# Kernel tuning notes

Measured on AMD Instinct MI355X. Metric: run time of the kernel, lower is better.

## Reference

```python
import jax, jax.numpy as jnp
import numpy as np

LAMBDA_INIT = 0.8
EPS = 1e-5


def setup_inputs() -> dict:
    key = jax.random.key(0)
    k1, k2, k3, k4 = jax.random.split(key, 4)
    B, H, S, D = 2, 16, 2048, 64
    return {
        "query": jax.random.normal(k1, (B, H, S, D), dtype=jnp.float32),
        "key": jax.random.normal(k2, (B, H, S, D), dtype=jnp.float32),
        "value": jax.random.normal(k3, (B, H, S, D), dtype=jnp.float32),
        "lambda_params": jax.random.uniform(k4, (H,), dtype=jnp.float32),
    }


def reference(query, key, value, lambda_params):
    # query/key/value: [B, H, S, D]; lambda_params: [H]
    B, H, S, D = query.shape
    d2 = D // 2
    scale = 1.0 / jnp.sqrt(jnp.float32(d2))
    q1, q2 = query[..., :d2], query[..., d2:]
    k1, k2 = key[..., :d2], key[..., d2:]
    # Two softmax attention maps over the split halves: [B, H, Sq, Sk]
    a1 = jax.nn.softmax(jnp.einsum("bhqd,bhkd->bhqk", q1, k1) * scale, axis=-1)
    a2 = jax.nn.softmax(jnp.einsum("bhqd,bhkd->bhqk", q2, k2) * scale, axis=-1)
    lam = lambda_params[None, :, None, None]  # [1, H, 1, 1]
    attn = a1 - lam * a2
    out = jnp.einsum("bhqk,bhkd->bhqd", attn, value)  # [B, H, S, D]
    # Groupnorm-style normalization per (batch, head, position) over head_dim,
    # then rescale by (1 - lambda_init).
    mean = jnp.mean(out, axis=-1, keepdims=True)
    var = jnp.mean(jnp.square(out - mean), axis=-1, keepdims=True)
    out = (out - mean) * jax.lax.rsqrt(var + EPS)
    out = out * (1.0 - LAMBDA_INIT)
    return out
```

## Files before the change

### kernel.cpp

```cpp
#include <hip/hip_runtime.h>

typedef __bf16 bf16x8 __attribute__((ext_vector_type(8)));
typedef float f32x4 __attribute__((ext_vector_type(4)));

static __device__ __forceinline__ f32x4 mfma16(bf16x8 a, bf16x8 b, f32x4 c) {
  return __builtin_amdgcn_mfma_f32_16x16x32_bf16(a, b, c, 0, 0, 0);
}
static __device__ __forceinline__ unsigned cvtpk(float lo, float hi) {
  unsigned r;
  asm("v_cvt_pk_bf16_f32 %0, %1, %2" : "=v"(r) : "v"(lo), "v"(hi));
  return r;
}

__global__ __launch_bounds__(256)
void kpack(const float* __restrict__ K, __bf16* __restrict__ KS) {
  const int bh = blockIdx.x >> 6, ch = blockIdx.x & 63;
  const int t = threadIdx.x;
  const int t2 = t >> 7, br = (t >> 6) & 1, g = (t >> 4) & 3, c = t & 15;
  const float* src = K + ((size_t)bh * 2048 + ch * 32 + t2 * 16 + c) * 64 + br * 32 + g * 8;
  float4 f0 = *(const float4*)src;
  float4 f1 = *(const float4*)(src + 4);
  bf16x8 v;
  v[0] = (__bf16)f0.x; v[1] = (__bf16)f0.y; v[2] = (__bf16)f0.z; v[3] = (__bf16)f0.w;
  v[4] = (__bf16)f1.x; v[5] = (__bf16)f1.y; v[6] = (__bf16)f1.z; v[7] = (__bf16)f1.w;
  *(bf16x8*)(KS + (size_t)bh * 131072 + ch * 2048 + t * 8) = v;
}

__global__ __launch_bounds__(256)
void vpack(const float* __restrict__ V, __bf16* __restrict__ VS) {
  __shared__ float tile[64][65];
  const int bh = blockIdx.x >> 5;
  const int s0 = (blockIdx.x & 31) * 64;
  const int t = threadIdx.x;
  const float* Vb = V + (size_t)bh * 2048 * 64;
#pragma unroll
  for (int i = 0; i < 4; ++i) {
    const int r = i * 16 + (t >> 4);
    const int c4 = (t & 15) * 4;
    float4 v = *(const float4*)(Vb + (s0 + r) * 64 + c4);
    tile[r][c4] = v.x; tile[r][c4 + 1] = v.y;
    tile[r][c4 + 2] = v.z; tile[r][c4 + 3] = v.w;
  }
  __syncthreads();
  const int dt = t >> 6, g = (t >> 4) & 3, c = t & 15;
#pragma unroll
  for (int h = 0; h < 2; ++h) {
    const int ch = (blockIdx.x & 31) * 2 + h;
    bf16x8 v;
#pragma unroll
    for (int j = 0; j < 8; ++j) v[j] = (__bf16)tile[h * 32 + 8 * g + j][16 * dt + c];
    *(bf16x8*)(VS + (size_t)bh * 131072 + ch * 2048 + dt * 512 + g * 128 + c * 8) = v;
  }
}

__global__ __launch_bounds__(256, 2)
void diffattn(const float* __restrict__ Q, const __bf16* __restrict__ KS,
              const __bf16* __restrict__ VS, const float* __restrict__ LP,
              float* __restrict__ OUT) {
  constexpr int S = 2048, D = 64;
  constexpr float QSCALE = 0.17677669529663687f * 1.4426950408889634f;

  __shared__ __align__(16) unsigned short Pl[4][2][16][40];

  const int raw = blockIdx.x;
  const int wg  = (raw & 7) * 64 + (raw >> 3);
  const int bh  = wg >> 4;
  const int qb  = wg & 15;
  const float lam = LP[bh & 15];

  const int tid  = threadIdx.x;
  const int w    = tid >> 6;
  const int lane = tid & 63;
  const int c    = lane & 15;
  const int g    = lane >> 4;
  const int q0   = qb * 128 + w * 32;

  const float*  Qb    = Q  + (size_t)bh * S * D;
  const __bf16* Kbase = KS + (size_t)bh * 131072 + g * 128 + c * 8;
  const __bf16* Vbase = VS + (size_t)bh * 131072 + g * 128 + c * 8;

  bf16x8 bq[2][2];
#pragma unroll
  for (int qt = 0; qt < 2; ++qt)
#pragma unroll
    for (int br = 0; br < 2; ++br) {
      const float* p = Qb + (q0 + qt * 16 + c) * D + br * 32 + 8 * g;
      float4 f0 = *(const float4*)p;
      float4 f1 = *(const float4*)(p + 4);
      bf16x8 v;
      v[0] = (__bf16)(f0.x * QSCALE); v[1] = (__bf16)(f0.y * QSCALE);
      v[2] = (__bf16)(f0.z * QSCALE); v[3] = (__bf16)(f0.w * QSCALE);
      v[4] = (__bf16)(f1.x * QSCALE); v[5] = (__bf16)(f1.y * QSCALE);
      v[6] = (__bf16)(f1.z * QSCALE); v[7] = (__bf16)(f1.w * QSCALE);
      bq[qt][br] = v;
    }

  f32x4 acc[2][2][4];
#pragma unroll
  for (int qt = 0; qt < 2; ++qt)
#pragma unroll
    for (int br = 0; br < 2; ++br)
#pragma unroll
      for (int dt = 0; dt < 4; ++dt)
        acc[qt][br][dt] = (f32x4){0.f, 0.f, 0.f, 0.f};
  float rsum[2][2] = {{0.f, 0.f}, {0.f, 0.f}};

#define LOADK(ak, ch) do {                                             \
    const __bf16* _p = Kbase + (size_t)(ch) * 2048;                    \
    ak[0][0] = *(const bf16x8*)_p;                                     \
    ak[0][1] = *(const bf16x8*)(_p + 512);                             \
    ak[1][0] = *(const bf16x8*)(_p + 1024);                            \
    ak[1][1] = *(const bf16x8*)(_p + 1536);                            \
  } while (0)

#define LOADV(av, ch) do {                                             \
    const __bf16* _p = Vbase + (size_t)(ch) * 2048;                    \
    _Pragma("unroll")                                                  \
    for (int dt = 0; dt < 4; ++dt)                                     \
      av[dt] = *(const bf16x8*)(_p + dt * 512);                        \
  } while (0)

#define STEP(akc, akn, avc, avn, ch) do {                                 \
    LOADK(akn, ((ch) + 1) & 63);                                          \
    LOADV(avn, ((ch) + 1) & 63);                                          \
    _Pragma("unroll")                                                     \
    for (int qt = 0; qt < 2; ++qt) {                                      \
      _Pragma("unroll")                                                   \
      for (int br = 0; br < 2; ++br) {                                    \
        f32x4 z = {0.f, 0.f, 0.f, 0.f};                                   \
        f32x4 sA = mfma16(akc[0][br], bq[qt][br], z);                     \
        f32x4 sB = mfma16(akc[1][br], bq[qt][br], z);                     \
        float pA[4], pB[4];                                               \
        _Pragma("unroll")                                                 \
        for (int r = 0; r < 4; ++r) {                                     \
          pA[r] = __builtin_amdgcn_exp2f(sA[r]);                          \
          pB[r] = __builtin_amdgcn_exp2f(sB[r]);                          \
        }                                                                 \
        rsum[qt][br] += (pA[0]+pA[1]+pA[2]+pA[3]) + (pB[0]+pB[1]+pB[2]+pB[3]); \
        uint2 uA; uA.x = cvtpk(pA[0], pA[1]); uA.y = cvtpk(pA[2], pA[3]); \
        uint2 uB; uB.x = cvtpk(pB[0], pB[1]); uB.y = cvtpk(pB[2], pB[3]); \
        *(uint2*)&Pl[w][br][c][4 * g]      = uA;                          \
        *(uint2*)&Pl[w][br][c][16 + 4 * g] = uB;                          \
      }                                                                   \
      __builtin_amdgcn_sched_barrier(0);   \
      _Pragma("unroll")                                                   \
      for (int br = 0; br < 2; ++br) {                                    \
        bf16x8 bp = *(const bf16x8*)&Pl[w][br][c][8 * g];                 \
        _Pragma("unroll")                                                 \
        for (int dt = 0; dt < 4; ++dt)                                    \
          acc[qt][br][dt] = mfma16(avc[dt], bp, acc[qt][br][dt]);         \
      }                                                                   \
      __builtin_amdgcn_sched_barrier(0);   \
    }                                                                     \
  } while (0)

  bf16x8 akA[2][2], akB[2][2], avA[4], avB[4];
  LOADK(akA, 0);
  LOADV(avA, 0);

#pragma unroll 1
  for (int ch = 0; ch < 64; ch += 2) {
    STEP(akA, akB, avA, avB, ch);
    STEP(akB, akA, avB, avA, ch + 1);
  }
#undef STEP
#undef LOADV
#undef LOADK

#pragma unroll
  for (int qt = 0; qt < 2; ++qt) {
    float rs1 = rsum[qt][0], rs2 = rsum[qt][1];
    rs1 += __shfl_xor(rs1, 16); rs1 += __shfl_xor(rs1, 32);
    rs2 += __shfl_xor(rs2, 16); rs2 += __shfl_xor(rs2, 32);
    const float inv1 = 1.0f / rs1;
    const float inv2 = lam / rs2;

    float vals[16];
    float sum = 0.f, sq = 0.f;
#pragma unroll
    for (int dt = 0; dt < 4; ++dt)
#pragma unroll
      for (int r = 0; r < 4; ++r) {
        float x = acc[qt][0][dt][r] * inv1 - acc[qt][1][dt][r] * inv2;
        vals[dt * 4 + r] = x;
        sum += x; sq += x * x;
      }
    sum += __shfl_xor(sum, 16); sum += __shfl_xor(sum, 32);
    sq  += __shfl_xor(sq, 16);  sq  += __shfl_xor(sq, 32);
    const float mean = sum * (1.0f / 64.0f);
    const float var  = sq * (1.0f / 64.0f) - mean * mean;
    const float rstd = rsqrtf(var + 1e-5f) * 0.2f;

    float* op = OUT + (size_t)bh * S * D + (size_t)(q0 + qt * 16 + c) * D;
#pragma unroll
    for (int dt = 0; dt < 4; ++dt) {
      float4 o;
      o.x = (vals[dt * 4 + 0] - mean) * rstd;
      o.y = (vals[dt * 4 + 1] - mean) * rstd;
      o.z = (vals[dt * 4 + 2] - mean) * rstd;
      o.w = (vals[dt * 4 + 3] - mean) * rstd;
      *(float4*)(op + 16 * dt + 4 * g) = o;
    }
  }
}

extern "C" void kernel_launch(void* const* d_in, const int* in_sizes, int n_in,
                              void* d_out, int out_size, void* d_ws, size_t ws_size,
                              hipStream_t stream) {
  (void)in_sizes; (void)n_in; (void)out_size; (void)ws_size;
  const float* q  = (const float*)d_in[0];
  const float* k  = (const float*)d_in[1];
  const float* v  = (const float*)d_in[2];
  const float* lp = (const float*)d_in[3];
  float* out = (float*)d_out;

  __bf16* ks = (__bf16*)d_ws;
  __bf16* vs = (__bf16*)((char*)d_ws + (8u << 20));

  kpack<<<dim3(2048), dim3(256), 0, stream>>>(k, ks);
  vpack<<<dim3(1024), dim3(256), 0, stream>>>(v, vs);
  diffattn<<<dim3(512), dim3(256), 0, stream>>>(q, ks, vs, lp, out);
}
```

Baseline: 79.17 us.

## Software-pipeline QK softmax and PV across chunks with double-buffered LDS

Restructures the main loop so the exp/pack of chunk n+1 is interleaved with the PV MFMAs of chunk n. P tiles go into a double-buffered LDS array indexed by parity, which removes the per-qt sched barriers and the write-then-read dependency inside a single step. K and V loads are reissued at different points to match the skewed schedule, with a prologue and an epilogue added. This raises LDS use and register pressure in exchange for better MFMA/VALU overlap.

```diff
diff --git a/kernel.cpp b/kernel.cpp
--- a/kernel.cpp
+++ b/kernel.cpp
@@ -60,7 +60,7 @@
   constexpr int S = 2048, D = 64;
   constexpr float QSCALE = 0.17677669529663687f * 1.4426950408889634f;
 
-  __shared__ __align__(16) unsigned short Pl[4][2][16][40];
+  __shared__ __align__(16) uint2 Pl[2][4][2][2][16][10];
 
   const int raw = blockIdx.x;
   const int wg  = (raw & 7) * 64 + (raw >> 3);
@@ -120,16 +120,14 @@
       av[dt] = *(const bf16x8*)(_p + dt * 512);                        \
   } while (0)
 
-#define STEP(akc, akn, avc, avn, ch) do {                                 \
-    LOADK(akn, ((ch) + 1) & 63);                                          \
-    LOADV(avn, ((ch) + 1) & 63);                                          \
+#define QKPACK(PW, kcur) do {                                             \
     _Pragma("unroll")                                                     \
-    for (int qt = 0; qt < 2; ++qt) {                                      \
+    for (int qt = 0; qt < 2; ++qt)                                        \
       _Pragma("unroll")                                                   \
       for (int br = 0; br < 2; ++br) {                                    \
         f32x4 z = {0.f, 0.f, 0.f, 0.f};                                   \
-        f32x4 sA = mfma16(akc[0][br], bq[qt][br], z);                     \
-        f32x4 sB = mfma16(akc[1][br], bq[qt][br], z);                     \
+        f32x4 sA = mfma16(kcur[0][br], bq[qt][br], z);                    \
+        f32x4 sB = mfma16(kcur[1][br], bq[qt][br], z);                    \
         float pA[4], pB[4];                                               \
         _Pragma("unroll")                                                 \
         for (int r = 0; r < 4; ++r) {                                     \
@@ -139,31 +137,66 @@
         rsum[qt][br] += (pA[0]+pA[1]+pA[2]+pA[3]) + (pB[0]+pB[1]+pB[2]+pB[3]); \
         uint2 uA; uA.x = cvtpk(pA[0], pA[1]); uA.y = cvtpk(pA[2], pA[3]); \
         uint2 uB; uB.x = cvtpk(pB[0], pB[1]); uB.y = cvtpk(pB[2], pB[3]); \
-        *(uint2*)&Pl[w][br][c][4 * g]      = uA;                          \
-        *(uint2*)&Pl[w][br][c][16 + 4 * g] = uB;                          \
+        Pl[PW][w][qt][br][c][g]     = uA;     \
+        Pl[PW][w][qt][br][c][4 + g] = uB;     \
       }                                                                   \
-      __builtin_amdgcn_sched_barrier(0);   \
+  } while (0)
+
+#define READP(pb, PR) do {                                                \
+    _Pragma("unroll")                                                     \
+    for (int qt = 0; qt < 2; ++qt)                                        \
       _Pragma("unroll")                                                   \
       for (int br = 0; br < 2; ++br) {                                    \
-        bf16x8 bp = *(const bf16x8*)&Pl[w][br][c][8 * g];                 \
+        uint2 lo = Pl[PR][w][qt][br][c][2 * g];                           \
+        uint2 hi = Pl[PR][w][qt][br][c][2 * g + 1];                       \
+        uint4 u = make_uint4(lo.x, lo.y, hi.x, hi.y);                     \
+        pb[qt][br] = __builtin_bit_cast(bf16x8, u);                       \
+      }                                                                   \
+  } while (0)
+
+#define STEP(PR, PW, kcur, knext, vprev, ch) do {                         \
+    bf16x8 pb[2][2];                                                      \
+    READP(pb, PR);                                                        \
+    LOADK(knext, ((ch) + 1) & 63);                                        \
+    QKPACK(PW, kcur);                                                     \
+    _Pragma("unroll")                                                     \
+    for (int qt = 0; qt < 2; ++qt)                                        \
+      _Pragma("unroll")                                                   \
+      for (int br = 0; br < 2; ++br)                                      \
         _Pragma("unroll")                                                 \
         for (int dt = 0; dt < 4; ++dt)                                    \
-          acc[qt][br][dt] = mfma16(avc[dt], bp, acc[qt][br][dt]);         \
-      }                                                                   \
-      __builtin_amdgcn_sched_barrier(0);   \
-    }                                                                     \
-  } while (0)
-
-  bf16x8 akA[2][2], akB[2][2], avA[4], avB[4];
-  LOADK(akA, 0);
-  LOADV(avA, 0);
+          acc[qt][br][dt] = mfma16(vprev[dt], pb[qt][br], acc[qt][br][dt]); \
+    LOADV(vprev, ((ch) + 1) & 63);                                        \
+    __builtin_amdgcn_sched_barrier(0);    \
+  } while (0)
+
+  bf16x8 k0[2][2], k1[2][2], v0[4], v1[4];
+  LOADK(k0, 0); LOADV(v0, 0);
+  LOADK(k1, 1); LOADV(v1, 1);
+  QKPACK(0, k0);
+  __builtin_amdgcn_sched_barrier(0);
 
 #pragma unroll 1
-  for (int ch = 0; ch < 64; ch += 2) {
-    STEP(akA, akB, avA, avB, ch);
-    STEP(akB, akA, avB, avA, ch + 1);
+  for (int c2 = 0; c2 < 31; ++c2) {
+    STEP(0, 1, k1, k0, v0, 2 * c2 + 1);
+    STEP(1, 0, k0, k1, v1, 2 * c2 + 2);
+  }
+  STEP(0, 1, k1, k0, v0, 63);
+
+  {
+    bf16x8 pb[2][2];
+    READP(pb, 1);
+#pragma unroll
+    for (int qt = 0; qt < 2; ++qt)
+#pragma unroll
+      for (int br = 0; br < 2; ++br)
+#pragma unroll
+        for (int dt = 0; dt < 4; ++dt)
+          acc[qt][br][dt] = mfma16(v1[dt], pb[qt][br], acc[qt][br][dt]);
   }
 #undef STEP
+#undef READP
+#undef QKPACK
 #undef LOADV
 #undef LOADK
 
```

Measured after the change: 77.13 us. 2.6% less time.

## Split key range across wave pairs and merge partial sums through shared memory

Applied to the files above, without the earlier changes.

Each workgroup now covers 64 queries instead of 128, and its four waves form two pairs that each process half of the key sequence. Partial accumulators and row sums from the second half are merged through LDS before normalization. The grid doubles to 1024 workgroups and the occupancy hint rises to 3 blocks per CU. The V prefetch is no longer double-buffered; it is issued after the current chunk's MFMAs. The design aims for more parallelism and occupancy, at the cost of an LDS reduction, barriers, and Q loads duplicated across the wave pairs.

```diff
diff --git a/kernel.cpp b/kernel.cpp
--- a/kernel.cpp
+++ b/kernel.cpp
@@ -44,40 +44,44 @@
   __syncthreads();
   const int dt = t >> 6, g = (t >> 4) & 3, c = t & 15;
 #pragma unroll
-  for (int h = 0; h < 2; ++h) {
-    const int ch = (blockIdx.x & 31) * 2 + h;
+  for (int hh = 0; hh < 2; ++hh) {
+    const int ch = (blockIdx.x & 31) * 2 + hh;
     bf16x8 v;
 #pragma unroll
-    for (int j = 0; j < 8; ++j) v[j] = (__bf16)tile[h * 32 + 8 * g + j][16 * dt + c];
+    for (int j = 0; j < 8; ++j) v[j] = (__bf16)tile[hh * 32 + 8 * g + j][16 * dt + c];
     *(bf16x8*)(VS + (size_t)bh * 131072 + ch * 2048 + dt * 512 + g * 128 + c * 8) = v;
   }
 }
 
-__global__ __launch_bounds__(256, 2)
+__global__ __launch_bounds__(256, 3)
 void diffattn(const float* __restrict__ Q, const __bf16* __restrict__ KS,
               const __bf16* __restrict__ VS, const float* __restrict__ LP,
               float* __restrict__ OUT) {
   constexpr int S = 2048, D = 64;
   constexpr float QSCALE = 0.17677669529663687f * 1.4426950408889634f;
 
-  __shared__ __align__(16) unsigned short Pl[4][2][16][40];
+  __shared__ __align__(16) uint2 Pl[4][2][2][16][10];
+  __shared__ __align__(16) f32x4 Macc[2][2][4][64];
+  __shared__ float Mrs[2][2][64];
 
   const int raw = blockIdx.x;
-  const int wg  = (raw & 7) * 64 + (raw >> 3);
-  const int bh  = wg >> 4;
-  const int qb  = wg & 15;
+  const int wg  = (raw & 7) * 128 + (raw >> 3);
+  const int bh  = wg >> 5;
+  const int qb  = wg & 31;
   const float lam = LP[bh & 15];
 
   const int tid  = threadIdx.x;
   const int w    = tid >> 6;
+  const int ws   = w & 1;
+  const int h    = w >> 1;
   const int lane = tid & 63;
   const int c    = lane & 15;
   const int g    = lane >> 4;
-  const int q0   = qb * 128 + w * 32;
+  const int q0   = qb * 64 + ws * 32;
 
   const float*  Qb    = Q  + (size_t)bh * S * D;
-  const __bf16* Kbase = KS + (size_t)bh * 131072 + g * 128 + c * 8;
-  const __bf16* Vbase = VS + (size_t)bh * 131072 + g * 128 + c * 8;
+  const __bf16* Kbase = KS + (size_t)bh * 131072 + h * 65536 + g * 128 + c * 8;
+  const __bf16* Vbase = VS + (size_t)bh * 131072 + h * 65536 + g * 128 + c * 8;
 
   bf16x8 bq[2][2];
 #pragma unroll
@@ -120,9 +124,8 @@
       av[dt] = *(const bf16x8*)(_p + dt * 512);                        \
   } while (0)
 
-#define STEP(akc, akn, avc, avn, ch) do {                                 \
-    LOADK(akn, ((ch) + 1) & 63);                                          \
-    LOADV(avn, ((ch) + 1) & 63);                                          \
+#define STEP(akc, akn, ch) do {                                           \
+    LOADK(akn, ((ch) + 1) & 31);                                          \
     _Pragma("unroll")                                                     \
     for (int qt = 0; qt < 2; ++qt) {                                      \
       _Pragma("unroll")                                                   \
@@ -139,29 +142,33 @@
         rsum[qt][br] += (pA[0]+pA[1]+pA[2]+pA[3]) + (pB[0]+pB[1]+pB[2]+pB[3]); \
         uint2 uA; uA.x = cvtpk(pA[0], pA[1]); uA.y = cvtpk(pA[2], pA[3]); \
         uint2 uB; uB.x = cvtpk(pB[0], pB[1]); uB.y = cvtpk(pB[2], pB[3]); \
-        *(uint2*)&Pl[w][br][c][4 * g]      = uA;                          \
-        *(uint2*)&Pl[w][br][c][16 + 4 * g] = uB;                          \
+        Pl[w][qt][br][c][g]     = uA;                                     \
+        Pl[w][qt][br][c][4 + g] = uB;                                     \
       }                                                                   \
-      __builtin_amdgcn_sched_barrier(0);   \
+      __builtin_amdgcn_sched_barrier(0);     \
       _Pragma("unroll")                                                   \
       for (int br = 0; br < 2; ++br) {                                    \
-        bf16x8 bp = *(const bf16x8*)&Pl[w][br][c][8 * g];                 \
+        uint2 lo = Pl[w][qt][br][c][2 * g];                               \
+        uint2 hi = Pl[w][qt][br][c][2 * g + 1];                           \
+        uint4 u = make_uint4(lo.x, lo.y, hi.x, hi.y);                     \
+        bf16x8 bp = __builtin_bit_cast(bf16x8, u);                        \
         _Pragma("unroll")                                                 \
         for (int dt = 0; dt < 4; ++dt)                                    \
-          acc[qt][br][dt] = mfma16(avc[dt], bp, acc[qt][br][dt]);         \
+          acc[qt][br][dt] = mfma16(av[dt], bp, acc[qt][br][dt]);          \
       }                                                                   \
-      __builtin_amdgcn_sched_barrier(0);   \
+      __builtin_amdgcn_sched_barrier(0);    \
     }                                                                     \
+    LOADV(av, ((ch) + 1) & 31);                                           \
   } while (0)
 
-  bf16x8 akA[2][2], akB[2][2], avA[4], avB[4];
-  LOADK(akA, 0);
-  LOADV(avA, 0);
+  bf16x8 k0[2][2], k1[2][2], av[4];
+  LOADK(k0, 0);
+  LOADV(av, 0);
 
 #pragma unroll 1
-  for (int ch = 0; ch < 64; ch += 2) {
-    STEP(akA, akB, avA, avB, ch);
-    STEP(akB, akA, avB, avA, ch + 1);
+  for (int ch = 0; ch < 32; ch += 2) {
+    STEP(k0, k1, ch);
+    STEP(k1, k0, ch + 1);
   }
 #undef STEP
 #undef LOADV
@@ -172,35 +179,58 @@
     float rs1 = rsum[qt][0], rs2 = rsum[qt][1];
     rs1 += __shfl_xor(rs1, 16); rs1 += __shfl_xor(rs1, 32);
     rs2 += __shfl_xor(rs2, 16); rs2 += __shfl_xor(rs2, 32);
-    const float inv1 = 1.0f / rs1;
-    const float inv2 = lam / rs2;
-
-    float vals[16];
-    float sum = 0.f, sq = 0.f;
-#pragma unroll
-    for (int dt = 0; dt < 4; ++dt)
-#pragma unroll
-      for (int r = 0; r < 4; ++r) {
-        float x = acc[qt][0][dt][r] * inv1 - acc[qt][1][dt][r] * inv2;
-        vals[dt * 4 + r] = x;
-        sum += x; sq += x * x;
+
+    if (h == 1) {
+#pragma unroll
+      for (int br = 0; br < 2; ++br)
+#pragma unroll
+        for (int dt = 0; dt < 4; ++dt)
+          Macc[ws][br][dt][lane] = acc[qt][br][dt];
+      Mrs[ws][0][lane] = rs1;
+      Mrs[ws][1][lane] = rs2;
+    }
+    __syncthreads();
+
+    if (h == 0) {
+      f32x4 a1[4], a2[4];
+#pragma unroll
+      for (int dt = 0; dt < 4; ++dt) {
+        a1[dt] = acc[qt][0][dt] + Macc[ws][0][dt][lane];
+        a2[dt] = acc[qt][1][dt] + Macc[ws][1][dt][lane];
       }
-    sum += __shfl_xor(sum, 16); sum += __shfl_xor(sum, 32);
-    sq  += __shfl_xor(sq, 16);  sq  += __shfl_xor(sq, 32);
-    const float mean = sum * (1.0f / 64.0f);
-    const float var  = sq * (1.0f / 64.0f) - mean * mean;
-    const float rstd = rsqrtf(var + 1e-5f) * 0.2f;
-
-    float* op = OUT + (size_t)bh * S * D + (size_t)(q0 + qt * 16 + c) * D;
-#pragma unroll
-    for (int dt = 0; dt < 4; ++dt) {
-      float4 o;
-      o.x = (vals[dt * 4 + 0] - mean) * rstd;
-      o.y = (vals[dt * 4 + 1] - mean) * rstd;
-      o.z = (vals[dt * 4 + 2] - mean) * rstd;
-      o.w = (vals[dt * 4 + 3] - mean) * rstd;
-      *(float4*)(op + 16 * dt + 4 * g) = o;
+      const float t1 = rs1 + Mrs[ws][0][lane];
+      const float t2 = rs2 + Mrs[ws][1][lane];
+      const float inv1 = 1.0f / t1;
+      const float inv2 = lam / t2;
+
+      float vals[16];
+      float sum = 0.f, sq = 0.f;
+#pragma unroll
+      for (int dt = 0; dt < 4; ++dt)
+#pragma unroll
+        for (int r = 0; r < 4; ++r) {
+          float x = a1[dt][r] * inv1 - a2[dt][r] * inv2;
+          vals[dt * 4 + r] = x;
+          sum += x; sq += x * x;
+        }
+      sum += __shfl_xor(sum, 16); sum += __shfl_xor(sum, 32);
+      sq  += __shfl_xor(sq, 16);  sq  += __shfl_xor(sq, 32);
+      const float mean = sum * (1.0f / 64.0f);
+      const float var  = sq * (1.0f / 64.0f) - mean * mean;
+      const float rstd = rsqrtf(var + 1e-5f) * 0.2f;
+
+      float* op = OUT + (size_t)bh * S * D + (size_t)(q0 + qt * 16 + c) * D;
+#pragma unroll
+      for (int dt = 0; dt < 4; ++dt) {
+        float4 o;
+        o.x = (vals[dt * 4 + 0] - mean) * rstd;
+        o.y = (vals[dt * 4 + 1] - mean) * rstd;
+        o.z = (vals[dt * 4 + 2] - mean) * rstd;
+        o.w = (vals[dt * 4 + 3] - mean) * rstd;
+        *(float4*)(op + 16 * dt + 4 * g) = o;
+      }
     }
+    __syncthreads();
   }
 }
 
@@ -219,5 +249,5 @@
 
   kpack<<<dim3(2048), dim3(256), 0, stream>>>(k, ks);
   vpack<<<dim3(1024), dim3(256), 0, stream>>>(v, vs);
-  diffattn<<<dim3(512), dim3(256), 0, stream>>>(q, ks, vs, lp, out);
-}
+  diffattn<<<dim3(1024), dim3(256), 0, stream>>>(q, ks, vs, lp, out);
+}
```

Measured after the change: 85.46 us. +7.9%, slower.

## Compute softmax row sums via MFMA with ones vector and batch P staging

Applied to the files above, without the earlier changes.

Removes the per-step scalar row-sum accumulation of exponentials and instead computes row sums with an extra MFMA against an all-ones bf16 operand, so the sums come out of the matrix unit. The P staging buffer is reshaped to hold both query tiles, letting all exp/store work for the two query tiles happen before a single barrier and then all PV MFMAs follow, which cuts the sched barriers per step from four to two. This trades VALU adds and end-of-loop shuffles for 25% more MFMAs, doubles the LDS used for P, and computes the sums from bf16-rounded probabilities rather than fp32 values.

```diff
diff --git a/kernel.cpp b/kernel.cpp
--- a/kernel.cpp
+++ b/kernel.cpp
@@ -44,11 +44,11 @@
   __syncthreads();
   const int dt = t >> 6, g = (t >> 4) & 3, c = t & 15;
 #pragma unroll
-  for (int h = 0; h < 2; ++h) {
-    const int ch = (blockIdx.x & 31) * 2 + h;
+  for (int hh = 0; hh < 2; ++hh) {
+    const int ch = (blockIdx.x & 31) * 2 + hh;
     bf16x8 v;
 #pragma unroll
-    for (int j = 0; j < 8; ++j) v[j] = (__bf16)tile[h * 32 + 8 * g + j][16 * dt + c];
+    for (int j = 0; j < 8; ++j) v[j] = (__bf16)tile[hh * 32 + 8 * g + j][16 * dt + c];
     *(bf16x8*)(VS + (size_t)bh * 131072 + ch * 2048 + dt * 512 + g * 128 + c * 8) = v;
   }
 }
@@ -60,7 +60,7 @@
   constexpr int S = 2048, D = 64;
   constexpr float QSCALE = 0.17677669529663687f * 1.4426950408889634f;
 
-  __shared__ __align__(16) unsigned short Pl[4][2][16][40];
+  __shared__ __align__(16) uint2 Pl[4][2][2][16][10];
 
   const int raw = blockIdx.x;
   const int wg  = (raw & 7) * 64 + (raw >> 3);
@@ -78,6 +78,12 @@
   const float*  Qb    = Q  + (size_t)bh * S * D;
   const __bf16* Kbase = KS + (size_t)bh * 131072 + g * 128 + c * 8;
   const __bf16* Vbase = VS + (size_t)bh * 131072 + g * 128 + c * 8;
+
+  bf16x8 aones;
+  {
+    uint4 u = make_uint4(0x3F803F80u, 0x3F803F80u, 0x3F803F80u, 0x3F803F80u);
+    aones = __builtin_bit_cast(bf16x8, u);
+  }
 
   bf16x8 bq[2][2];
 #pragma unroll
@@ -95,15 +101,14 @@
       bq[qt][br] = v;
     }
 
-  f32x4 acc[2][2][4];
+  f32x4 acc[2][2][5];
 #pragma unroll
   for (int qt = 0; qt < 2; ++qt)
 #pragma unroll
     for (int br = 0; br < 2; ++br)
 #pragma unroll
-      for (int dt = 0; dt < 4; ++dt)
+      for (int dt = 0; dt < 5; ++dt)
         acc[qt][br][dt] = (f32x4){0.f, 0.f, 0.f, 0.f};
-  float rsum[2][2] = {{0.f, 0.f}, {0.f, 0.f}};
 
 #define LOADK(ak, ch) do {                                             \
     const __bf16* _p = Kbase + (size_t)(ch) * 2048;                    \
@@ -123,8 +128,9 @@
 #define STEP(akc, akn, avc, avn, ch) do {                                 \
     LOADK(akn, ((ch) + 1) & 63);                                          \
     LOADV(avn, ((ch) + 1) & 63);                                          \
+     \
     _Pragma("unroll")                                                     \
-    for (int qt = 0; qt < 2; ++qt) {                                      \
+    for (int qt = 0; qt < 2; ++qt)                                        \
       _Pragma("unroll")                                                   \
       for (int br = 0; br < 2; ++br) {                                    \
         f32x4 z = {0.f, 0.f, 0.f, 0.f};                                   \
@@ -136,32 +142,37 @@
           pA[r] = __builtin_amdgcn_exp2f(sA[r]);                          \
           pB[r] = __builtin_amdgcn_exp2f(sB[r]);                          \
         }                                                                 \
-        rsum[qt][br] += (pA[0]+pA[1]+pA[2]+pA[3]) + (pB[0]+pB[1]+pB[2]+pB[3]); \
         uint2 uA; uA.x = cvtpk(pA[0], pA[1]); uA.y = cvtpk(pA[2], pA[3]); \
         uint2 uB; uB.x = cvtpk(pB[0], pB[1]); uB.y = cvtpk(pB[2], pB[3]); \
-        *(uint2*)&Pl[w][br][c][4 * g]      = uA;                          \
-        *(uint2*)&Pl[w][br][c][16 + 4 * g] = uB;                          \
+        Pl[w][qt][br][c][g]     = uA;                                     \
+        Pl[w][qt][br][c][4 + g] = uB;                                     \
       }                                                                   \
-      __builtin_amdgcn_sched_barrier(0);   \
+    __builtin_amdgcn_sched_barrier(0);       \
+             \
+    _Pragma("unroll")                                                     \
+    for (int qt = 0; qt < 2; ++qt)                                        \
       _Pragma("unroll")                                                   \
       for (int br = 0; br < 2; ++br) {                                    \
-        bf16x8 bp = *(const bf16x8*)&Pl[w][br][c][8 * g];                 \
+        uint2 lo = Pl[w][qt][br][c][2 * g];                               \
+        uint2 hi = Pl[w][qt][br][c][2 * g + 1];                           \
+        uint4 u = make_uint4(lo.x, lo.y, hi.x, hi.y);                     \
+        bf16x8 bp = __builtin_bit_cast(bf16x8, u);                        \
         _Pragma("unroll")                                                 \
         for (int dt = 0; dt < 4; ++dt)                                    \
           acc[qt][br][dt] = mfma16(avc[dt], bp, acc[qt][br][dt]);         \
+        acc[qt][br][4] = mfma16(aones, bp, acc[qt][br][4]);               \
       }                                                                   \
-      __builtin_amdgcn_sched_barrier(0);   \
-    }                                                                     \
+    __builtin_amdgcn_sched_barrier(0);   \
   } while (0)
 
-  bf16x8 akA[2][2], akB[2][2], avA[4], avB[4];
-  LOADK(akA, 0);
-  LOADV(avA, 0);
+  bf16x8 k0[2][2], k1[2][2], v0[4], v1[4];
+  LOADK(k0, 0);
+  LOADV(v0, 0);
 
 #pragma unroll 1
   for (int ch = 0; ch < 64; ch += 2) {
-    STEP(akA, akB, avA, avB, ch);
-    STEP(akB, akA, avB, avA, ch + 1);
+    STEP(k0, k1, v0, v1, ch);
+    STEP(k1, k0, v1, v0, ch + 1);
   }
 #undef STEP
 #undef LOADV
@@ -169,11 +180,8 @@
 
 #pragma unroll
   for (int qt = 0; qt < 2; ++qt) {
-    float rs1 = rsum[qt][0], rs2 = rsum[qt][1];
-    rs1 += __shfl_xor(rs1, 16); rs1 += __shfl_xor(rs1, 32);
-    rs2 += __shfl_xor(rs2, 16); rs2 += __shfl_xor(rs2, 32);
-    const float inv1 = 1.0f / rs1;
-    const float inv2 = lam / rs2;
+    const float inv1 = 1.0f / acc[qt][0][4][0];
+    const float inv2 = lam / acc[qt][1][4][0];
 
     float vals[16];
     float sum = 0.f, sq = 0.f;
```

New measurement: 76.00 us. 1.04x faster.
